# Optimization experiments

Measured on AMD Instinct MI355X. Metric: run time of the kernel, lower is better.

Reference implementation:

```python
import jax, jax.numpy as jnp
import numpy as np

B, S, D, H = 4, 2048, 512, 8
HD = D // H  # 64


def setup_inputs() -> dict:
    key = jax.random.key(0)
    ks = jax.random.split(key, 7)
    scale = 1.0 / np.sqrt(D)
    return {
        "query": jax.random.normal(ks[0], (B, S, D), jnp.float32),
        "key": jax.random.normal(ks[1], (B, S, D), jnp.float32),
        "value": jax.random.normal(ks[2], (B, S, D), jnp.float32),
        # Only the `query` Linear and fc_out are actually used in the original forward
        "Wq": jax.random.uniform(ks[3], (D, D), jnp.float32, -scale, scale),
        "bq": jnp.zeros((D,), jnp.float32),
        "Wo": jax.random.uniform(ks[4], (D, D), jnp.float32, -scale, scale),
        "bo": jnp.zeros((D,), jnp.float32),
    }


def reference(query, key, value, Wq, bq, Wo, bo):
    # Faithful to source: Q, K, V all use the *query* projection (bug preserved)
    def proj(x):
        # [B,S,D] -> [B,H,S,HD]
        y = x @ Wq + bq
        return y.reshape(B, S, H, HD).transpose(0, 2, 1, 3)

    Q, K, V = proj(query), proj(key), proj(value)
    scores = jnp.einsum("bhqd,bhkd->bhqk", Q, K) / jnp.sqrt(jnp.float32(HD))
    attn = jax.nn.softmax(scores, axis=-1)
    x = jnp.einsum("bhqk,bhkd->bhqd", attn, V)
    x = x.transpose(0, 2, 1, 3).reshape(B, S, D)
    return x @ Wo + bo
```

## Files before the change

### kernel.cpp

```cpp
#include <hip/hip_runtime.h>
#include <math.h>

#define B_ 4
#define S_ 2048
#define D_ 512
#define H_ 8
#define HD_ 64
#define SZ_ (B_ * S_ * D_)
#define WSZ_ (D_ * D_)
#define BSH_ (B_ * S_ * H_)

#define QSCALE_ 0.18033688011112042f

typedef _Float16 v4h __attribute__((ext_vector_type(4)));
typedef _Float16 v8h __attribute__((ext_vector_type(8)));
typedef float    v4f __attribute__((ext_vector_type(4)));

__device__ __forceinline__ void gload16(const void* g, void* l) {
    __builtin_amdgcn_global_load_lds((__attribute__((address_space(1))) void*)g,
                                     (__attribute__((address_space(3))) void*)l,
                                     16, 0, 0);
}

__device__ __forceinline__ v8h pack8(v4f a, v4f b) {
    return __builtin_shufflevector(__builtin_convertvector(a, v4h),
                                   __builtin_convertvector(b, v4h),
                                   0, 1, 2, 3, 4, 5, 6, 7);
}

__global__ __launch_bounds__(256) void wtrans_kernel(const float* __restrict__ Wq,
                                                     const float* __restrict__ Wo,
                                                     _Float16* __restrict__ Wt) {
    __shared__ float Ts[64][132];
    const int kc = blockIdx.x, nt = blockIdx.y, mat = blockIdx.z;
    const float* W = mat ? Wo : Wq;
    const int k0 = kc * 64, n0 = nt * 128;
    const int t = threadIdx.x;
#pragma unroll
    for (int i = 0; i < 8; i++) {
        int s2 = t + i * 256;
        int kk = s2 >> 5, nc = (s2 & 31) * 4;
        *(float4*)&Ts[kk][nc] = *(const float4*)&W[(size_t)(k0 + kk) * 512 + n0 + nc];
    }
    __syncthreads();
    _Float16* blk = Wt + (((size_t)mat * 4 + nt) * 8 + kc) * 8192;
#pragma unroll
    for (int i = 0; i < 4; i++) {
        int s2 = t + i * 256;
        int r = s2 >> 3, s = s2 & 7;
        int kl = (s ^ (r & 7)) * 8;
        v8h p;
#pragma unroll
        for (int j = 0; j < 8; j++) p[j] = (_Float16)Ts[kl + j][r];
        *(v8h*)&blk[r * 64 + s * 8] = p;
    }
}

__global__ __launch_bounds__(256) void proj_mfma(const float* __restrict__ q,
                                                 const float* __restrict__ kin,
                                                 const float* __restrict__ v,
                                                 const _Float16* __restrict__ Wt,
                                                 const float* __restrict__ bq,
                                                 _Float16* __restrict__ Qh,
                                                 _Float16* __restrict__ Kh,
                                                 _Float16* __restrict__ VT) {
    __shared__ __align__(16) _Float16 As[2][8192];
    __shared__ __align__(16) _Float16 Bs[2][8192];
    const int blk = blockIdx.x;
    const int wl = (blk & 7) * 96 + (blk >> 3);
    const int z = wl >> 8;
    const int rem = wl & 255;
    const int mt = rem >> 2, nt = rem & 3;
    const int n0 = nt * 128, m0 = mt * 128;
    const float* X = (z == 0) ? q : ((z == 1) ? kin : v);
    const int t = threadIdx.x, lane = t & 63, w = t >> 6;
    const int wm = w >> 1, wn = w & 1;
    const int quad = lane >> 4, l16 = lane & 15;

    const float* Ap[4];
    int wofs[4];
#pragma unroll
    for (int i = 0; i < 4; i++) {
        int s2 = t + i * 256;
        int r = s2 >> 3, c = s2 & 7;
        Ap[i] = X + (size_t)(m0 + r) * 512 + c * 8;
        wofs[i] = r * 64 + ((c ^ (r & 7)) * 8);
    }
    const _Float16* Bb = Wt + ((size_t)nt * 8) * 8192 + w * 512 + lane * 8;

    v4f acc[4][4];
#pragma unroll
    for (int mi = 0; mi < 4; mi++)
#pragma unroll
        for (int ni = 0; ni < 4; ni++) acc[mi][ni] = (v4f)0.f;

    v4f a0[4], a1[4];
#pragma unroll
    for (int i = 0; i < 4; i++) {
        a0[i] = *(const v4f*)(Ap[i]);
        a1[i] = *(const v4f*)(Ap[i] + 4);
    }
#pragma unroll
    for (int i = 0; i < 4; i++) *(v8h*)&As[0][wofs[i]] = pack8(a0[i], a1[i]);
#pragma unroll
    for (int i = 0; i < 4; i++)
        gload16(Bb + i * 2048, &Bs[0][w * 512 + i * 2048]);
#pragma unroll
    for (int i = 0; i < 4; i++) {
        a0[i] = *(const v4f*)(Ap[i] + 64);
        a1[i] = *(const v4f*)(Ap[i] + 68);
    }
    __syncthreads();

    int cur = 0;
    for (int kc = 0; kc < 8; ++kc) {
        const int nxt = cur ^ 1;
        if (kc + 1 < 8) {
#pragma unroll
            for (int i = 0; i < 4; i++) *(v8h*)&As[nxt][wofs[i]] = pack8(a0[i], a1[i]);
#pragma unroll
            for (int i = 0; i < 4; i++)
                gload16(Bb + (kc + 1) * 8192 + i * 2048, &Bs[nxt][w * 512 + i * 2048]);
        }
        if (kc + 2 < 8) {
#pragma unroll
            for (int i = 0; i < 4; i++) {
                a0[i] = *(const v4f*)(Ap[i] + (kc + 2) * 64);
                a1[i] = *(const v4f*)(Ap[i] + (kc + 2) * 64 + 4);
            }
        }

#pragma unroll
        for (int ks = 0; ks < 2; ++ks) {
            const int sxx = (ks * 32 + quad * 8) ^ ((l16 & 7) * 8);
            v8h af[4], bf[4];
#pragma unroll
            for (int mi = 0; mi < 4; mi++)
                af[mi] = *(const v8h*)&As[cur][(wm * 64 + mi * 16 + l16) * 64 + sxx];
#pragma unroll
            for (int ni = 0; ni < 4; ni++)
                bf[ni] = *(const v8h*)&Bs[cur][(wn * 64 + ni * 16 + l16) * 64 + sxx];
#pragma unroll
            for (int mi = 0; mi < 4; mi++)
#pragma unroll
                for (int ni = 0; ni < 4; ni++)
                    acc[mi][ni] = __builtin_amdgcn_mfma_f32_16x16x32_f16(af[mi], bf[ni], acc[mi][ni], 0, 0, 0);
        }
        __syncthreads();
        cur = nxt;
    }

    if (z < 2) {
        _Float16* Y = z ? Kh : Qh;
        const float sc = z ? 1.f : QSCALE_;
#pragma unroll
        for (int mi = 0; mi < 4; mi++) {
            int mb = m0 + wm * 64 + mi * 16 + quad * 4;
#pragma unroll
            for (int ni = 0; ni < 4; ni++) {
                int n = n0 + wn * 64 + ni * 16 + l16;
                float bj = bq[n];
#pragma unroll
                for (int r = 0; r < 4; r++)
                    Y[(size_t)(mb + r) * 512 + n] = (_Float16)((acc[mi][ni][r] + bj) * sc);
            }
        }
    } else {
#pragma unroll
        for (int mi = 0; mi < 4; mi++) {
            int tile0 = (m0 & 2047) + wm * 64;
            int pos = tile0 + (mi >> 1) * 32 + quad * 8 + (mi & 1) * 4;
            int b = m0 >> 11;
#pragma unroll
            for (int ni = 0; ni < 4; ni++) {
                int n = n0 + wn * 64 + ni * 16 + l16;
                int h = n >> 6, dd = n & 63;
                float bj = bq[n];
                v4h pk;
#pragma unroll
                for (int r = 0; r < 4; r++) pk[r] = (_Float16)(acc[mi][ni][r] + bj);
                *(v4h*)&VT[(((size_t)b * H_ + h) * HD_ + dd) * S_ + pos] = pk;
            }
        }
    }
}

__global__ __launch_bounds__(256) void outproj_mfma(const _Float16* __restrict__ Ah,
                                                    const _Float16* __restrict__ Wt,
                                                    const float* __restrict__ bo,
                                                    float* __restrict__ out) {
    __shared__ __align__(16) _Float16 As[2][8192];
    __shared__ __align__(16) _Float16 Bs[2][8192];
    const int blk = blockIdx.x;
    const int wl = (blk & 7) * 32 + (blk >> 3);
    const int mt = wl >> 2, nt = wl & 3;
    const int n0 = nt * 128, m0 = mt * 128;
    const int t = threadIdx.x, lane = t & 63, w = t >> 6;
    const int wm = w >> 1, wn = w & 1;
    const int quad = lane >> 4, l16 = lane & 15;

    const _Float16* Ab = Ah + ((size_t)mt * 8) * 8192 + w * 512 + lane * 8;
    const _Float16* Bb = Wt + (size_t)(4 + nt) * 8 * 8192 + w * 512 + lane * 8;

    v4f acc[4][4];
#pragma unroll
    for (int mi = 0; mi < 4; mi++)
#pragma unroll
        for (int ni = 0; ni < 4; ni++) acc[mi][ni] = (v4f)0.f;

#pragma unroll
    for (int i = 0; i < 4; i++) {
        gload16(Ab + i * 2048, &As[0][w * 512 + i * 2048]);
        gload16(Bb + i * 2048, &Bs[0][w * 512 + i * 2048]);
    }
    __syncthreads();

    int cur = 0;
    for (int kc = 0; kc < 8; ++kc) {
        const int nxt = cur ^ 1;
        if (kc + 1 < 8) {
#pragma unroll
            for (int i = 0; i < 4; i++) {
                gload16(Ab + (kc + 1) * 8192 + i * 2048, &As[nxt][w * 512 + i * 2048]);
                gload16(Bb + (kc + 1) * 8192 + i * 2048, &Bs[nxt][w * 512 + i * 2048]);
            }
        }

#pragma unroll
        for (int ks = 0; ks < 2; ++ks) {
            const int sxx = (ks * 32 + quad * 8) ^ ((l16 & 7) * 8);
            v8h af[4], bf[4];
#pragma unroll
            for (int mi = 0; mi < 4; mi++)
                af[mi] = *(const v8h*)&As[cur][(wm * 64 + mi * 16 + l16) * 64 + sxx];
#pragma unroll
            for (int ni = 0; ni < 4; ni++)
                bf[ni] = *(const v8h*)&Bs[cur][(wn * 64 + ni * 16 + l16) * 64 + sxx];
#pragma unroll
            for (int mi = 0; mi < 4; mi++)
#pragma unroll
                for (int ni = 0; ni < 4; ni++)
                    acc[mi][ni] = __builtin_amdgcn_mfma_f32_16x16x32_f16(af[mi], bf[ni], acc[mi][ni], 0, 0, 0);
        }
        __syncthreads();
        cur = nxt;
    }

#pragma unroll
    for (int mi = 0; mi < 4; mi++) {
        int mb = m0 + wm * 64 + mi * 16 + quad * 4;
#pragma unroll
        for (int ni = 0; ni < 4; ni++) {
            int n = n0 + wn * 64 + ni * 16 + l16;
            float bj = bo[n];
#pragma unroll
            for (int r = 0; r < 4; r++)
                out[(size_t)(mb + r) * 512 + n] = acc[mi][ni][r] + bj;
        }
    }
}

__global__ __launch_bounds__(256) void flash_attn_f16(const _Float16* __restrict__ Qh,
                                                      const _Float16* __restrict__ Kh,
                                                      const _Float16* __restrict__ VT,
                                                      _Float16* __restrict__ Ah) {
    __shared__ _Float16 Ks[128 * 72];
    __shared__ _Float16 Vs[64 * 136];

    const int t     = threadIdx.x;
    const int lane  = t & 63;
    const int w     = t >> 6;
    const int quad  = lane >> 4;
    const int l16   = lane & 15;
    const int blk = blockIdx.x;
    const int xcd = blk & 7, idx = blk >> 3;
    const int pid = xcd * 4 + (idx >> 4);
    const int qb  = idx & 15;
    const int b   = pid >> 3, h = pid & 7;
    const int q0  = qb * 128;

    const size_t base  = (size_t)b * S_ * D_ + (size_t)h * HD_;
    const size_t vbase = ((size_t)b * H_ + h) * HD_ * (size_t)S_;

    v8h qf[2][2];
#pragma unroll
    for (int nb = 0; nb < 2; nb++) {
        const _Float16* qrow = Qh + base + (size_t)(q0 + w * 32 + nb * 16 + l16) * D_;
        qf[nb][0] = *(const v8h*)(qrow + quad * 8);
        qf[nb][1] = *(const v8h*)(qrow + 32 + quad * 8);
    }

    v4f o[2][4];
#pragma unroll
    for (int nb = 0; nb < 2; nb++)
#pragma unroll
        for (int i = 0; i < 4; i++) o[nb][i] = (v4f)0.f;
    float l_lane[2] = {0.f, 0.f};

    v8h kv[4], vv[4];
#define LOADKV(kk)                                                             \
    do {                                                                       \
        _Pragma("unroll") for (int i = 0; i < 4; i++) {                        \
            int c = t + i * 256;                                               \
            kv[i] = *(const v8h*)(Kh + base + (size_t)((kk) + (c >> 3)) * D_ + (c & 7) * 8); \
            vv[i] = *(const v8h*)(VT + vbase + (size_t)(c >> 4) * S_ + (kk) + (c & 15) * 8); \
        }                                                                      \
    } while (0)

    LOADKV(0);

    for (int kk0 = 0; kk0 < S_; kk0 += 128) {
        __syncthreads();
#pragma unroll
        for (int i = 0; i < 4; i++) {
            int c = t + i * 256;
            *(v8h*)&Ks[(c >> 3) * 72 + (c & 7) * 8] = kv[i];
            *(v8h*)&Vs[(c >> 4) * 136 + (c & 15) * 8] = vv[i];
        }
        __syncthreads();

        if (kk0 + 128 < S_) LOADKV(kk0 + 128);

#pragma unroll
        for (int hh = 0; hh < 2; hh++) {
            v4f sc[4][2];
#pragma unroll
            for (int mb = 0; mb < 4; mb++)
#pragma unroll
                for (int nb = 0; nb < 2; nb++) sc[mb][nb] = (v4f)0.f;
#pragma unroll
            for (int ks = 0; ks < 2; ks++) {
#pragma unroll
                for (int mb = 0; mb < 4; mb++) {
                    v8h ak = *(const v8h*)&Ks[(hh * 64 + mb * 16 + l16) * 72 + ks * 32 + quad * 8];
#pragma unroll
                    for (int nb = 0; nb < 2; nb++)
                        sc[mb][nb] = __builtin_amdgcn_mfma_f32_16x16x32_f16(ak, qf[nb][ks], sc[mb][nb], 0, 0, 0);
                }
            }

            v4h pf[4][2];
#pragma unroll
            for (int nb = 0; nb < 2; nb++) {
#pragma unroll
                for (int mb = 0; mb < 4; mb++) {
                    v4f pv;
#pragma unroll
                    for (int r = 0; r < 4; r++) pv[r] = __builtin_amdgcn_exp2f(sc[mb][nb][r]);
                    pf[mb][nb] = __builtin_convertvector(pv, v4h);
                    l_lane[nb] += (pv[0] + pv[1]) + (pv[2] + pv[3]);
                }
            }

#pragma unroll
            for (int p = 0; p < 2; p++) {
#pragma unroll
                for (int dblk = 0; dblk < 4; dblk++) {
                    v8h vf2 = *(const v8h*)&Vs[(dblk * 16 + l16) * 136 + hh * 64 + p * 32 + quad * 8];
                    v4h vlo = __builtin_shufflevector(vf2, vf2, 0, 1, 2, 3);
                    v4h vhi = __builtin_shufflevector(vf2, vf2, 4, 5, 6, 7);
#pragma unroll
                    for (int nb = 0; nb < 2; nb++) {
                        o[nb][dblk] = __builtin_amdgcn_mfma_f32_16x16x16f16(vlo, pf[2 * p][nb], o[nb][dblk], 0, 0, 0);
                        o[nb][dblk] = __builtin_amdgcn_mfma_f32_16x16x16f16(vhi, pf[2 * p + 1][nb], o[nb][dblk], 0, 0, 0);
                    }
                }
            }
        }
    }
#undef LOADKV

#pragma unroll
    for (int nb = 0; nb < 2; nb++) {
        float rs = l_lane[nb];
        rs += __shfl_xor(rs, 16);
        rs += __shfl_xor(rs, 32);
        float linv = __builtin_amdgcn_rcpf(rs);
        int r = w * 32 + nb * 16 + l16;
        _Float16* blkp = Ah + (((size_t)(b * 16 + qb)) * 8 + h) * 8192 + r * 64;
#pragma unroll
        for (int dblk = 0; dblk < 4; dblk++) {
            int s = dblk * 2 + (quad >> 1);
            v4h pk;
#pragma unroll
            for (int rr = 0; rr < 4; rr++) pk[rr] = (_Float16)(o[nb][dblk][rr] * linv);
            *(v4h*)&blkp[((s ^ (r & 7)) * 8) + (quad & 1) * 4] = pk;
        }
    }
}

extern "C" void kernel_launch(void* const* d_in, const int* in_sizes, int n_in,
                              void* d_out, int out_size, void* d_ws, size_t ws_size,
                              hipStream_t stream) {
    const float* query = (const float*)d_in[0];
    const float* key   = (const float*)d_in[1];
    const float* value = (const float*)d_in[2];
    const float* Wq    = (const float*)d_in[3];
    const float* bq    = (const float*)d_in[4];
    const float* Wo    = (const float*)d_in[5];
    const float* bo    = (const float*)d_in[6];
    float* out = (float*)d_out;

    _Float16* ws = (_Float16*)d_ws;
    _Float16* Qh = ws;
    _Float16* Kh = ws + (size_t)SZ_;
    _Float16* VT = ws + 2 * (size_t)SZ_;
    _Float16* Wt = ws + 3 * (size_t)SZ_;
    _Float16* Ah = ws + 3 * (size_t)SZ_ + 2 * (size_t)WSZ_;

    wtrans_kernel<<<dim3(8, 4, 2), 256, 0, stream>>>(Wq, Wo, Wt);
    proj_mfma<<<dim3(768), 256, 0, stream>>>(query, key, value, Wt, bq, Qh, Kh, VT);
    flash_attn_f16<<<dim3(512), 256, 0, stream>>>(Qh, Kh, VT, Ah);
    outproj_mfma<<<dim3(256), 256, 0, stream>>>(Ah, Wt, bo, out);
}
```

Baseline: 186.5 us.

## Split key halves across two wave groups in flash attention with LDS reduction

Doubles the flash attention block to 512 threads so each half of the waves handles one 64-key half of every 128-key tile, rather than each wave looping over both halves. The partial outputs and row sums are combined through shared memory at the end, with one group writing and the other summing and storing. This cuts the serial work per wave and raises the number of waves in flight to hide MFMA and exp latency. In exchange it adds an end-of-kernel LDS reduction, extra barriers, and higher register and LDS pressure per block.

```diff
diff --git a/kernel.cpp b/kernel.cpp
--- a/kernel.cpp
+++ b/kernel.cpp
@@ -260,16 +260,21 @@
     }
 }
 
-__global__ __launch_bounds__(256) void flash_attn_f16(const _Float16* __restrict__ Qh,
+__global__ __launch_bounds__(512) void flash_attn_f16(const _Float16* __restrict__ Qh,
                                                       const _Float16* __restrict__ Kh,
                                                       const _Float16* __restrict__ VT,
                                                       _Float16* __restrict__ Ah) {
-    __shared__ _Float16 Ks[128 * 72];
-    __shared__ _Float16 Vs[64 * 136];
+    __shared__ __align__(16) unsigned char smem[35840];
+    _Float16* Ks = (_Float16*)smem;
+    _Float16* Vs = (_Float16*)(smem + 18432);
+    float* obuf = (float*)smem;
+    float* lbuf = (float*)(smem + 34816);
 
     const int t     = threadIdx.x;
     const int lane  = t & 63;
     const int w     = t >> 6;
+    const int wq    = w & 3;
+    const int hh    = w >> 2;
     const int quad  = lane >> 4;
     const int l16   = lane & 15;
     const int blk = blockIdx.x;
@@ -285,7 +290,7 @@
     v8h qf[2][2];
 #pragma unroll
     for (int nb = 0; nb < 2; nb++) {
-        const _Float16* qrow = Qh + base + (size_t)(q0 + w * 32 + nb * 16 + l16) * D_;
+        const _Float16* qrow = Qh + base + (size_t)(q0 + wq * 32 + nb * 16 + l16) * D_;
         qf[nb][0] = *(const v8h*)(qrow + quad * 8);
         qf[nb][1] = *(const v8h*)(qrow + 32 + quad * 8);
     }
@@ -297,11 +302,11 @@
         for (int i = 0; i < 4; i++) o[nb][i] = (v4f)0.f;
     float l_lane[2] = {0.f, 0.f};
 
-    v8h kv[4], vv[4];
+    v8h kv[2], vv[2];
 #define LOADKV(kk)                                                             \
     do {                                                                       \
-        _Pragma("unroll") for (int i = 0; i < 4; i++) {                        \
-            int c = t + i * 256;                                               \
+        _Pragma("unroll") for (int i = 0; i < 2; i++) {                        \
+            int c = t + i * 512;                                               \
             kv[i] = *(const v8h*)(Kh + base + (size_t)((kk) + (c >> 3)) * D_ + (c & 7) * 8); \
             vv[i] = *(const v8h*)(VT + vbase + (size_t)(c >> 4) * S_ + (kk) + (c & 15) * 8); \
         }                                                                      \
@@ -312,8 +317,8 @@
     for (int kk0 = 0; kk0 < S_; kk0 += 128) {
         __syncthreads();
 #pragma unroll
-        for (int i = 0; i < 4; i++) {
-            int c = t + i * 256;
+        for (int i = 0; i < 2; i++) {
+            int c = t + i * 512;
             *(v8h*)&Ks[(c >> 3) * 72 + (c & 7) * 8] = kv[i];
             *(v8h*)&Vs[(c >> 4) * 136 + (c & 15) * 8] = vv[i];
         }
@@ -321,70 +326,88 @@
 
         if (kk0 + 128 < S_) LOADKV(kk0 + 128);
 
-#pragma unroll
-        for (int hh = 0; hh < 2; hh++) {
-            v4f sc[4][2];
-#pragma unroll
-            for (int mb = 0; mb < 4; mb++)
-#pragma unroll
-                for (int nb = 0; nb < 2; nb++) sc[mb][nb] = (v4f)0.f;
-#pragma unroll
-            for (int ks = 0; ks < 2; ks++) {
-#pragma unroll
-                for (int mb = 0; mb < 4; mb++) {
-                    v8h ak = *(const v8h*)&Ks[(hh * 64 + mb * 16 + l16) * 72 + ks * 32 + quad * 8];
-#pragma unroll
-                    for (int nb = 0; nb < 2; nb++)
-                        sc[mb][nb] = __builtin_amdgcn_mfma_f32_16x16x32_f16(ak, qf[nb][ks], sc[mb][nb], 0, 0, 0);
+        v4f sc[4][2];
+#pragma unroll
+        for (int mb = 0; mb < 4; mb++)
+#pragma unroll
+            for (int nb = 0; nb < 2; nb++) sc[mb][nb] = (v4f)0.f;
+#pragma unroll
+        for (int ks = 0; ks < 2; ks++) {
+#pragma unroll
+            for (int mb = 0; mb < 4; mb++) {
+                v8h ak = *(const v8h*)&Ks[(hh * 64 + mb * 16 + l16) * 72 + ks * 32 + quad * 8];
+#pragma unroll
+                for (int nb = 0; nb < 2; nb++)
+                    sc[mb][nb] = __builtin_amdgcn_mfma_f32_16x16x32_f16(ak, qf[nb][ks], sc[mb][nb], 0, 0, 0);
+            }
+        }
+
+        v4h pf[4][2];
+#pragma unroll
+        for (int nb = 0; nb < 2; nb++) {
+#pragma unroll
+            for (int mb = 0; mb < 4; mb++) {
+                v4f pv;
+#pragma unroll
+                for (int r = 0; r < 4; r++) pv[r] = __builtin_amdgcn_exp2f(sc[mb][nb][r]);
+                pf[mb][nb] = __builtin_convertvector(pv, v4h);
+                l_lane[nb] += (pv[0] + pv[1]) + (pv[2] + pv[3]);
+            }
+        }
+
+#pragma unroll
+        for (int p = 0; p < 2; p++) {
+#pragma unroll
+            for (int dblk = 0; dblk < 4; dblk++) {
+                v8h vf2 = *(const v8h*)&Vs[(dblk * 16 + l16) * 136 + hh * 64 + p * 32 + quad * 8];
+                v4h vlo = __builtin_shufflevector(vf2, vf2, 0, 1, 2, 3);
+                v4h vhi = __builtin_shufflevector(vf2, vf2, 4, 5, 6, 7);
+#pragma unroll
+                for (int nb = 0; nb < 2; nb++) {
+                    o[nb][dblk] = __builtin_amdgcn_mfma_f32_16x16x16f16(vlo, pf[2 * p][nb], o[nb][dblk], 0, 0, 0);
+                    o[nb][dblk] = __builtin_amdgcn_mfma_f32_16x16x16f16(vhi, pf[2 * p + 1][nb], o[nb][dblk], 0, 0, 0);
                 }
             }
-
-            v4h pf[4][2];
-#pragma unroll
-            for (int nb = 0; nb < 2; nb++) {
-#pragma unroll
-                for (int mb = 0; mb < 4; mb++) {
-                    v4f pv;
-#pragma unroll
-                    for (int r = 0; r < 4; r++) pv[r] = __builtin_amdgcn_exp2f(sc[mb][nb][r]);
-                    pf[mb][nb] = __builtin_convertvector(pv, v4h);
-                    l_lane[nb] += (pv[0] + pv[1]) + (pv[2] + pv[3]);
-                }
-            }
-
-#pragma unroll
-            for (int p = 0; p < 2; p++) {
-#pragma unroll
-                for (int dblk = 0; dblk < 4; dblk++) {
-                    v8h vf2 = *(const v8h*)&Vs[(dblk * 16 + l16) * 136 + hh * 64 + p * 32 + quad * 8];
-                    v4h vlo = __builtin_shufflevector(vf2, vf2, 0, 1, 2, 3);
-                    v4h vhi = __builtin_shufflevector(vf2, vf2, 4, 5, 6, 7);
-#pragma unroll
-                    for (int nb = 0; nb < 2; nb++) {
-                        o[nb][dblk] = __builtin_amdgcn_mfma_f32_16x16x16f16(vlo, pf[2 * p][nb], o[nb][dblk], 0, 0, 0);
-                        o[nb][dblk] = __builtin_amdgcn_mfma_f32_16x16x16f16(vhi, pf[2 * p + 1][nb], o[nb][dblk], 0, 0, 0);
-                    }
-                }
-            }
         }
     }
 #undef LOADKV
 
+    __syncthreads();
+    float rs[2];
+    int rl[2];
 #pragma unroll
     for (int nb = 0; nb < 2; nb++) {
-        float rs = l_lane[nb];
-        rs += __shfl_xor(rs, 16);
-        rs += __shfl_xor(rs, 32);
-        float linv = __builtin_amdgcn_rcpf(rs);
-        int r = w * 32 + nb * 16 + l16;
-        _Float16* blkp = Ah + (((size_t)(b * 16 + qb)) * 8 + h) * 8192 + r * 64;
-#pragma unroll
-        for (int dblk = 0; dblk < 4; dblk++) {
-            int s = dblk * 2 + (quad >> 1);
-            v4h pk;
-#pragma unroll
-            for (int rr = 0; rr < 4; rr++) pk[rr] = (_Float16)(o[nb][dblk][rr] * linv);
-            *(v4h*)&blkp[((s ^ (r & 7)) * 8) + (quad & 1) * 4] = pk;
+        float r0 = l_lane[nb];
+        r0 += __shfl_xor(r0, 16);
+        r0 += __shfl_xor(r0, 32);
+        rs[nb] = r0;
+        rl[nb] = wq * 32 + nb * 16 + l16;
+    }
+    if (hh == 0) {
+#pragma unroll
+        for (int nb = 0; nb < 2; nb++) {
+            if (quad == 0) lbuf[rl[nb]] = rs[nb];
+#pragma unroll
+            for (int dblk = 0; dblk < 4; dblk++)
+                *(v4f*)&obuf[rl[nb] * 68 + dblk * 16 + quad * 4] = o[nb][dblk];
+        }
+    }
+    __syncthreads();
+    if (hh == 1) {
+#pragma unroll
+        for (int nb = 0; nb < 2; nb++) {
+            float linv = __builtin_amdgcn_rcpf(rs[nb] + lbuf[rl[nb]]);
+            int r = rl[nb];
+            _Float16* blkp = Ah + (((size_t)(b * 16 + qb)) * 8 + h) * 8192 + r * 64;
+#pragma unroll
+            for (int dblk = 0; dblk < 4; dblk++) {
+                v4f osum = o[nb][dblk] + *(const v4f*)&obuf[r * 68 + dblk * 16 + quad * 4];
+                int s = dblk * 2 + (quad >> 1);
+                v4h pk;
+#pragma unroll
+                for (int rr = 0; rr < 4; rr++) pk[rr] = (_Float16)(osum[rr] * linv);
+                *(v4h*)&blkp[((s ^ (r & 7)) * 8) + (quad & 1) * 4] = pk;
+            }
         }
     }
 }
@@ -410,6 +433,6 @@
 
     wtrans_kernel<<<dim3(8, 4, 2), 256, 0, stream>>>(Wq, Wo, Wt);
     proj_mfma<<<dim3(768), 256, 0, stream>>>(query, key, value, Wt, bq, Qh, Kh, VT);
-    flash_attn_f16<<<dim3(512), 256, 0, stream>>>(Qh, Kh, VT, Ah);
+    flash_attn_f16<<<dim3(512), 512, 0, stream>>>(Qh, Kh, VT, Ah);
     outproj_mfma<<<dim3(256), 256, 0, stream>>>(Ah, Wt, bo, out);
 }
```

Measured after the change: 185.8 us. No clear change (-0.4%).
